# Kernel tuning notes

Measured on AMD Instinct MI355X. Metric: run time of the kernel, lower is better.

Reference implementation:

```python
import jax, jax.numpy as jnp
import numpy as np

BAND_WIDTHS = [16]*20 + [32]*12 + [64]*4 + [65]
B, C, F, T, E = 4, 2, 1025, 2048, 128
MAX_BW = 65
D = C * MAX_BW * 2  # padded feature dim (in_channels * max_bandwidth * reim)
EPS = 1e-5


def _band_meta():
    widths = np.asarray(BAND_WIDTHS, np.int32)
    starts = np.concatenate([[0], np.cumsum(widths)[:-1]]).astype(np.int32)
    nb = len(widths)
    bw_mask = (np.arange(MAX_BW)[None, :] < widths[:, None])  # [nb, MAX_BW]
    # feature order per band is (channel, bw, reim), matching torch view_as_real+reshape
    feat_mask = np.broadcast_to(bw_mask[:, None, :, None], (nb, C, MAX_BW, 2)).reshape(nb, D)
    return starts, widths, feat_mask.astype(np.float32)


def setup_inputs() -> dict:
    key = jax.random.key(0)
    ks = jax.random.split(key, 6)
    starts, widths, feat_mask = _band_meta()
    nb = len(widths)
    fm = jnp.asarray(feat_mask)
    x = jax.random.normal(ks[0], (B, C, F, T, 2), jnp.float32)
    ln_gamma = (1.0 + 0.1 * jax.random.normal(ks[1], (nb, D), jnp.float32)) * fm
    ln_beta = 0.1 * jax.random.normal(ks[2], (nb, D), jnp.float32) * fm
    v = 0.05 * jax.random.normal(ks[3], (nb, E, D), jnp.float32) * fm[:, None, :]
    g = 1.0 + 0.1 * jax.random.normal(ks[4], (nb, E), jnp.float32)
    bias = 0.05 * jax.random.normal(ks[5], (nb, E), jnp.float32)
    return {
        "x": x, "ln_gamma": ln_gamma, "ln_beta": ln_beta, "v": v, "g": g,
        "bias": bias, "band_start": jnp.asarray(starts), "band_width": jnp.asarray(widths),
    }


def reference(x, ln_gamma, ln_beta, v, g, bias, band_start, band_width):
    nb = band_start.shape[0]
    # padded gather of each band's frequency slice
    idx = jnp.clip(band_start[:, None] + jnp.arange(MAX_BW)[None, :], 0, F - 1)  # [nb, MAX_BW]
    xb = jnp.take(x, idx, axis=2)               # [B, C, nb, MAX_BW, T, 2]
    xb = jnp.transpose(xb, (0, 2, 4, 1, 3, 5))  # [B, nb, T, C, MAX_BW, 2]
    xb = xb.reshape(B, nb, T, D)
    bw_mask = (jnp.arange(MAX_BW)[None, :] < band_width[:, None])
    fm = jnp.broadcast_to(bw_mask[:, None, :, None], (nb, C, MAX_BW, 2)).reshape(nb, D).astype(x.dtype)
    m = fm[None, :, None, :]                    # [1, nb, 1, D]
    n = (band_width * C * 2).astype(x.dtype)[None, :, None]  # true norm_in per band
    # masked LayerNorm over the valid (ragged) features of each band
    mean = jnp.sum(xb * m, axis=-1) / n         # [B, nb, T]
    diff = (xb - mean[..., None]) * m
    var = jnp.sum(diff * diff, axis=-1) / n
    xhat = diff * jax.lax.rsqrt(var + EPS)[..., None]
    y = (xhat * ln_gamma[None, :, None, :] + ln_beta[None, :, None, :]) * m
    # weight-normalized Linear: W = g * V / ||V||_row (padded cols of V are zero)
    vnorm = jnp.sqrt(jnp.sum(v * v, axis=-1, keepdims=True))  # [nb, E, 1]
    W = g[..., None] * v / vnorm
    z = jnp.einsum("bntd,ned->bnte", y, W) + bias[:, None, :]  # [B, nb, T, E]
    return z
```

## Files before the change

### kernel.cpp

```cpp
#include <hip/hip_runtime.h>
#include <math.h>

#define NB 37
#define BB 4
#define CC 2
#define FF 1025
#define TT 2048
#define EE 128
#define DD 260
#define EPSF 1e-5f
#define CHS 9

typedef short s16x8 __attribute__((ext_vector_type(8)));
typedef float f32x4 __attribute__((ext_vector_type(4)));

__device__ __forceinline__ unsigned short f2bf(float f) {
    unsigned u = __builtin_bit_cast(unsigned, f);
    unsigned r = (u + 0x7FFFu + ((u >> 16) & 1u)) >> 16;
    return (unsigned short)r;
}

__global__ __launch_bounds__(256) void prep_kernel(
    const float* __restrict__ gamma, const float* __restrict__ beta,
    const float* __restrict__ v, const float* __restrict__ g,
    const float* __restrict__ bias, const int* __restrict__ bwidth,
    unsigned short* __restrict__ ATg, float* __restrict__ s1o, float* __restrict__ s2o)
{
    int bid = blockIdx.x;
    int n   = bid >> 4;
    int eg  = bid & 15;
    int tid = threadIdx.x;
    int el  = tid >> 5;
    int kk  = tid & 31;
    int e   = eg * 8 + el;

    int bw    = bwidth[n];
    int Deff  = 4 * bw;
    int twobw = 2 * bw;
    int nCh   = (Deff + 31) >> 5;

    const float* vp = v + (size_t)(n * EE + e) * DD;

    float sq = 0.f;
    for (int d = kk; d < DD; d += 32) { float val = vp[d]; sq = fmaf(val, val, sq); }
    #pragma unroll
    for (int m = 16; m >= 1; m >>= 1) sq += __shfl_xor(sq, m);

    float rv = g[n * EE + e] * rsqrtf(sq);

    float s1 = 0.f, s2 = 0.f;
    unsigned short* Abase = ATg + (size_t)n * CHS * (EE * 32) + e * 32 + kk;
    for (int ch = 0; ch < nCh; ++ch) {
        int k = ch * 32 + kk;
        float a = 0.f;
        if (k < Deff) {
            int d = (k >= twobw) ? (130 + k - twobw) : k;
            float W = rv * vp[d];
            a = gamma[n * DD + d] * W;
            s1 += a;
            s2 = fmaf(beta[n * DD + d], W, s2);
        }
        Abase[(size_t)ch * (EE * 32)] = f2bf(a);
    }
    #pragma unroll
    for (int m = 16; m >= 1; m >>= 1) { s1 += __shfl_xor(s1, m); s2 += __shfl_xor(s2, m); }
    if (kk == 0) {
        s1o[n * EE + e] = s1;
        s2o[n * EE + e] = s2 + bias[n * EE + e];
    }
}

template <bool PRED>
__device__ __forceinline__ void do_chunk(
    const float* __restrict__ xt, const unsigned* offP,
    const s16x8* __restrict__ Ab, int ch, int nPairs, int ksub,
    f32x4 (&acc)[4][4], float (&sA)[4], float (&qA)[4])
{
    s16x8 bfr[4];
    #pragma unroll
    for (int ni = 0; ni < 4; ++ni) bfr[ni] = Ab[ch * 512 + ni * 64];

    int pb = ch * 16 + (ksub << 2);
    unsigned o[4]; bool val[4];
    #pragma unroll
    for (int j = 0; j < 4; ++j) {
        int p = pb + j;
        val[j] = !PRED || (p < nPairs);
        o[j] = offP[p];
    }

    #pragma unroll
    for (int mi = 0; mi < 4; ++mi) {
        float2 vv[4];
        #pragma unroll
        for (int j = 0; j < 4; ++j) {
            vv[j] = make_float2(0.f, 0.f);
            if (val[j])
                vv[j] = *reinterpret_cast<const float2*>(xt + o[j] + mi * 32);
        }
        float s = sA[mi], q = qA[mi];
        #pragma unroll
        for (int j = 0; j < 4; ++j) {
            s += vv[j].x + vv[j].y;
            q = fmaf(vv[j].x, vv[j].x, q);
            q = fmaf(vv[j].y, vv[j].y, q);
        }
        sA[mi] = s; qA[mi] = q;
        s16x8 af;
        #pragma unroll
        for (int j = 0; j < 4; ++j) {
            af[2 * j]     = (short)f2bf(vv[j].x);
            af[2 * j + 1] = (short)f2bf(vv[j].y);
        }
        #pragma unroll
        for (int ni = 0; ni < 4; ++ni)
            acc[mi][ni] = __builtin_amdgcn_mfma_f32_16x16x32_bf16(
                af, bfr[ni], acc[mi][ni], 0, 0, 0);
    }
}

__global__ __launch_bounds__(256) void fused_kernel(
    const float* __restrict__ x, const int* __restrict__ bstart,
    const int* __restrict__ bwidth,
    const unsigned short* __restrict__ ATg, const float* __restrict__ s1a,
    const float* __restrict__ s2a, float* __restrict__ out)
{
    int bid = blockIdx.x;
    int tt  = bid & 15;
    int n   = (bid >> 4) % NB;
    int b   = bid / (16 * NB);
    int t0  = tt * 128;
    int f0  = bstart[n];
    int bw  = bwidth[n];
    int nPairs = 2 * bw;
    int Deff   = 4 * bw;

    int tid  = threadIdx.x;
    int lane = tid & 63;
    int l15  = lane & 15;
    int ksub = lane >> 4;

    __shared__ unsigned offP[CHS * 16];

    if (tid < CHS * 16) {
        unsigned off = 0;
        if (tid < nPairs) {
            int c = (tid >= bw) ? 1 : 0;
            int w = tid - c * bw;
            off = (unsigned)(((b * CC + c) * FF + f0 + w) * (TT * 2));
        }
        offP[tid] = off;
    }
    __syncthreads();

    int wv    = tid >> 6;
    int twave = t0 + (wv >> 1) * 64;
    int ewave = (wv & 1) * 64;

    f32x4 acc[4][4];
    #pragma unroll
    for (int mi = 0; mi < 4; ++mi)
        #pragma unroll
        for (int ni = 0; ni < 4; ++ni)
            acc[mi][ni] = (f32x4){0.f, 0.f, 0.f, 0.f};
    float sA[4] = {0.f, 0.f, 0.f, 0.f};
    float qA[4] = {0.f, 0.f, 0.f, 0.f};

    const float* xt = x + (size_t)(twave + l15) * 2;
    const s16x8* Ab = reinterpret_cast<const s16x8*>(
        ATg + (size_t)n * CHS * (EE * 32) + ((ewave + l15) * 32 + ksub * 8));

    int nChF = Deff >> 5;
    int rem  = Deff & 31;

    for (int ch = 0; ch < nChF; ++ch)
        do_chunk<false>(xt, offP, Ab, ch, nPairs, ksub, acc, sA, qA);
    if (rem)
        do_chunk<true>(xt, offP, Ab, nChF, nPairs, ksub, acc, sA, qA);

    float inv = 1.f / (float)Deff;
    float mrow[4][4], rrow[4][4];
    #pragma unroll
    for (int mi = 0; mi < 4; ++mi) {
        float s = sA[mi], q = qA[mi];
        s += __shfl_xor(s, 16); s += __shfl_xor(s, 32);
        q += __shfl_xor(q, 16); q += __shfl_xor(q, 32);
        float mean = s * inv;
        float var  = fmaf(q, inv, -mean * mean);
        float rs   = rsqrtf(var + EPSF);
        #pragma unroll
        for (int j = 0; j < 4; ++j) {
            int src = (ksub << 2) + j;
            mrow[mi][j] = __shfl(mean, src);
            rrow[mi][j] = __shfl(rs, src);
        }
    }

    float s1r[4], s2r[4];
    #pragma unroll
    for (int ni = 0; ni < 4; ++ni) {
        int e = ewave + ni * 16 + l15;
        s1r[ni] = s1a[n * EE + e];
        s2r[ni] = s2a[n * EE + e];
    }
    size_t outRow = ((size_t)(b * NB + n)) * TT;
    #pragma unroll
    for (int mi = 0; mi < 4; ++mi) {
        #pragma unroll
        for (int j = 0; j < 4; ++j) {
            int t = twave + mi * 16 + (ksub << 2) + j;
            float m = mrow[mi][j], r = rrow[mi][j];
            float* op = out + (outRow + t) * EE + ewave + l15;
            #pragma unroll
            for (int ni = 0; ni < 4; ++ni)
                op[ni * 16] = fmaf(r, acc[mi][ni][j] - m * s1r[ni], s2r[ni]);
        }
    }
}

extern "C" void kernel_launch(void* const* d_in, const int* in_sizes, int n_in,
                              void* d_out, int out_size, void* d_ws, size_t ws_size,
                              hipStream_t stream)
{
    const float* x      = (const float*)d_in[0];
    const float* gamma  = (const float*)d_in[1];
    const float* beta   = (const float*)d_in[2];
    const float* v      = (const float*)d_in[3];
    const float* g      = (const float*)d_in[4];
    const float* bias   = (const float*)d_in[5];
    const int*   bstart = (const int*)d_in[6];
    const int*   bwidth = (const int*)d_in[7];
    float* out = (float*)d_out;

    unsigned short* ATg = (unsigned short*)d_ws;
    float* s1  = (float*)(ATg + (size_t)NB * CHS * EE * 32);
    float* s2p = s1 + NB * EE;

    prep_kernel<<<NB * 16, 256, 0, stream>>>(gamma, beta, v, g, bias, bwidth, ATg, s1, s2p);
    fused_kernel<<<BB * NB * 16, 256, 0, stream>>>(x, bstart, bwidth, ATg, s1, s2p, out);
}
```

Before: 94.23 us.

## Specialize fused kernel per band width with double-buffered register prefetch

The fused kernel now dispatches to a template instantiated for each band width (16, 32, 64, 65), so the chunk count is a compile-time constant and the chunk loop is fully unrolled. Input and weight fragments for the next chunk are loaded into a second register buffer while the current chunk is computed, so global-memory latency overlaps the MFMAs. The shared-memory offset table and its barrier are replaced by offsets computed directly from the band start. The cost is higher register pressure from two fragment buffers, which could lower occupancy, plus larger code from four instantiations. The else branch assumes every other band is width 65, which matches the task's band list.

```diff
diff --git a/kernel.cpp b/kernel.cpp
--- a/kernel.cpp
+++ b/kernel.cpp
@@ -70,52 +70,140 @@
     }
 }
 
-template <bool PRED>
-__device__ __forceinline__ void do_chunk(
-    const float* __restrict__ xt, const unsigned* offP,
-    const s16x8* __restrict__ Ab, int ch, int nPairs, int ksub,
-    f32x4 (&acc)[4][4], float (&sA)[4], float (&qA)[4])
-{
-    s16x8 bfr[4];
-    #pragma unroll
-    for (int ni = 0; ni < 4; ++ni) bfr[ni] = Ab[ch * 512 + ni * 64];
-
-    int pb = ch * 16 + (ksub << 2);
-    unsigned o[4]; bool val[4];
+struct Frag {
+    float2 xv[16];
+    s16x8  a[4];
+};
+
+template <int BW>
+__device__ __forceinline__ void load_chunk(
+    int ch, bool tailch, const char* __restrict__ xb,
+    const s16x8* __restrict__ Ab, int ksub, Frag& f)
+{
+    #pragma unroll
+    for (int ni = 0; ni < 4; ++ni)
+        f.a[ni] = Ab[ch * 512 + ni * 64];
+
     #pragma unroll
     for (int j = 0; j < 4; ++j) {
-        int p = pb + j;
-        val[j] = !PRED || (p < nPairs);
-        o[j] = offP[p];
-    }
-
+        int p = ch * 16 + ksub * 4 + j;
+        const char* ap = xb + (size_t)p * 16384
+                       + ((p >= BW) ? (size_t)(FF - BW) * 16384 : (size_t)0);
+        bool valid = !tailch || (ksub * 4 + j) < (2 * BW - ch * 16);
+        #pragma unroll
+        for (int mi = 0; mi < 4; ++mi) {
+            float2 vv = make_float2(0.f, 0.f);
+            if (valid)
+                vv = *reinterpret_cast<const float2*>(ap + mi * 128);
+            f.xv[j * 4 + mi] = vv;
+        }
+    }
+}
+
+__device__ __forceinline__ void compute_chunk(
+    const Frag& f, f32x4 (&acc)[4][4], float (&sA)[4], float (&qA)[4])
+{
     #pragma unroll
     for (int mi = 0; mi < 4; ++mi) {
-        float2 vv[4];
+        float s = 0.f, q = 0.f;
+        s16x8 af;
         #pragma unroll
         for (int j = 0; j < 4; ++j) {
-            vv[j] = make_float2(0.f, 0.f);
-            if (val[j])
-                vv[j] = *reinterpret_cast<const float2*>(xt + o[j] + mi * 32);
-        }
-        float s = sA[mi], q = qA[mi];
-        #pragma unroll
-        for (int j = 0; j < 4; ++j) {
-            s += vv[j].x + vv[j].y;
-            q = fmaf(vv[j].x, vv[j].x, q);
-            q = fmaf(vv[j].y, vv[j].y, q);
-        }
-        sA[mi] = s; qA[mi] = q;
-        s16x8 af;
-        #pragma unroll
-        for (int j = 0; j < 4; ++j) {
-            af[2 * j]     = (short)f2bf(vv[j].x);
-            af[2 * j + 1] = (short)f2bf(vv[j].y);
-        }
+            float2 vv = f.xv[j * 4 + mi];
+            s += vv.x + vv.y;
+            q = fmaf(vv.x, vv.x, q);
+            q = fmaf(vv.y, vv.y, q);
+            af[2 * j]     = (short)f2bf(vv.x);
+            af[2 * j + 1] = (short)f2bf(vv.y);
+        }
+        sA[mi] += s;
+        qA[mi] += q;
         #pragma unroll
         for (int ni = 0; ni < 4; ++ni)
             acc[mi][ni] = __builtin_amdgcn_mfma_f32_16x16x32_bf16(
-                af, bfr[ni], acc[mi][ni], 0, 0, 0);
+                af, f.a[ni], acc[mi][ni], 0, 0, 0);
+    }
+}
+
+template <int BW, bool TAIL>
+__device__ __forceinline__ void run_band(
+    const float* __restrict__ x, const unsigned short* __restrict__ ATg,
+    const float* __restrict__ s1a, const float* __restrict__ s2a,
+    float* __restrict__ out, int b, int n, int t0, int f0, int tid)
+{
+    constexpr int NCHF = (4 * BW) / 32;
+    constexpr int NCH  = NCHF + (TAIL ? 1 : 0);
+
+    int lane = tid & 63;
+    int l15  = lane & 15;
+    int ksub = lane >> 4;
+    int wv    = tid >> 6;
+    int twave = t0 + (wv >> 1) * 64;
+    int ewave = (wv & 1) * 64;
+
+    const char* xb = (const char*)x
+        + ((size_t)(b * 2 * FF + f0)) * 16384
+        + (size_t)(twave + l15) * 8;
+    const s16x8* Ab = reinterpret_cast<const s16x8*>(
+        ATg + (size_t)n * CHS * (EE * 32)) + ((ewave + l15) * 4 + ksub);
+
+    f32x4 acc[4][4];
+    #pragma unroll
+    for (int mi = 0; mi < 4; ++mi)
+        #pragma unroll
+        for (int ni = 0; ni < 4; ++ni)
+            acc[mi][ni] = (f32x4){0.f, 0.f, 0.f, 0.f};
+    float sA[4] = {0.f, 0.f, 0.f, 0.f};
+    float qA[4] = {0.f, 0.f, 0.f, 0.f};
+
+    Frag fr0, fr1;
+    load_chunk<BW>(0, false, xb, Ab, ksub, fr0);
+    #pragma unroll
+    for (int ch = 0; ch < NCH; ++ch) {
+        Frag& cur = (ch & 1) ? fr1 : fr0;
+        Frag& nxt = (ch & 1) ? fr0 : fr1;
+        if (ch + 1 < NCH)
+            load_chunk<BW>(ch + 1, (ch + 1 == NCHF) && TAIL, xb, Ab, ksub, nxt);
+        compute_chunk(cur, acc, sA, qA);
+    }
+
+    constexpr float inv = 1.f / (float)(4 * BW);
+    float mrow[4][4], rrow[4][4];
+    #pragma unroll
+    for (int mi = 0; mi < 4; ++mi) {
+        float s = sA[mi], q = qA[mi];
+        s += __shfl_xor(s, 16); s += __shfl_xor(s, 32);
+        q += __shfl_xor(q, 16); q += __shfl_xor(q, 32);
+        float mean = s * inv;
+        float var  = fmaf(q, inv, -mean * mean);
+        float rs   = rsqrtf(var + EPSF);
+        #pragma unroll
+        for (int j = 0; j < 4; ++j) {
+            int src = (ksub << 2) + j;
+            mrow[mi][j] = __shfl(mean, src);
+            rrow[mi][j] = __shfl(rs, src);
+        }
+    }
+
+    float s1r[4], s2r[4];
+    #pragma unroll
+    for (int ni = 0; ni < 4; ++ni) {
+        int e = ewave + ni * 16 + l15;
+        s1r[ni] = s1a[n * EE + e];
+        s2r[ni] = s2a[n * EE + e];
+    }
+    size_t outRow = ((size_t)(b * NB + n)) * TT;
+    #pragma unroll
+    for (int mi = 0; mi < 4; ++mi) {
+        #pragma unroll
+        for (int j = 0; j < 4; ++j) {
+            int t = twave + mi * 16 + (ksub << 2) + j;
+            float m = mrow[mi][j], r = rrow[mi][j];
+            float* op = out + (outRow + t) * EE + ewave + l15;
+            #pragma unroll
+            for (int ni = 0; ni < 4; ++ni)
+                op[ni * 16] = fmaf(r, acc[mi][ni][j] - m * s1r[ni], s2r[ni]);
+        }
     }
 }
 
@@ -132,90 +220,16 @@
     int t0  = tt * 128;
     int f0  = bstart[n];
     int bw  = bwidth[n];
-    int nPairs = 2 * bw;
-    int Deff   = 4 * bw;
-
-    int tid  = threadIdx.x;
-    int lane = tid & 63;
-    int l15  = lane & 15;
-    int ksub = lane >> 4;
-
-    __shared__ unsigned offP[CHS * 16];
-
-    if (tid < CHS * 16) {
-        unsigned off = 0;
-        if (tid < nPairs) {
-            int c = (tid >= bw) ? 1 : 0;
-            int w = tid - c * bw;
-            off = (unsigned)(((b * CC + c) * FF + f0 + w) * (TT * 2));
-        }
-        offP[tid] = off;
-    }
-    __syncthreads();
-
-    int wv    = tid >> 6;
-    int twave = t0 + (wv >> 1) * 64;
-    int ewave = (wv & 1) * 64;
-
-    f32x4 acc[4][4];
-    #pragma unroll
-    for (int mi = 0; mi < 4; ++mi)
-        #pragma unroll
-        for (int ni = 0; ni < 4; ++ni)
-            acc[mi][ni] = (f32x4){0.f, 0.f, 0.f, 0.f};
-    float sA[4] = {0.f, 0.f, 0.f, 0.f};
-    float qA[4] = {0.f, 0.f, 0.f, 0.f};
-
-    const float* xt = x + (size_t)(twave + l15) * 2;
-    const s16x8* Ab = reinterpret_cast<const s16x8*>(
-        ATg + (size_t)n * CHS * (EE * 32) + ((ewave + l15) * 32 + ksub * 8));
-
-    int nChF = Deff >> 5;
-    int rem  = Deff & 31;
-
-    for (int ch = 0; ch < nChF; ++ch)
-        do_chunk<false>(xt, offP, Ab, ch, nPairs, ksub, acc, sA, qA);
-    if (rem)
-        do_chunk<true>(xt, offP, Ab, nChF, nPairs, ksub, acc, sA, qA);
-
-    float inv = 1.f / (float)Deff;
-    float mrow[4][4], rrow[4][4];
-    #pragma unroll
-    for (int mi = 0; mi < 4; ++mi) {
-        float s = sA[mi], q = qA[mi];
-        s += __shfl_xor(s, 16); s += __shfl_xor(s, 32);
-        q += __shfl_xor(q, 16); q += __shfl_xor(q, 32);
-        float mean = s * inv;
-        float var  = fmaf(q, inv, -mean * mean);
-        float rs   = rsqrtf(var + EPSF);
-        #pragma unroll
-        for (int j = 0; j < 4; ++j) {
-            int src = (ksub << 2) + j;
-            mrow[mi][j] = __shfl(mean, src);
-            rrow[mi][j] = __shfl(rs, src);
-        }
-    }
-
-    float s1r[4], s2r[4];
-    #pragma unroll
-    for (int ni = 0; ni < 4; ++ni) {
-        int e = ewave + ni * 16 + l15;
-        s1r[ni] = s1a[n * EE + e];
-        s2r[ni] = s2a[n * EE + e];
-    }
-    size_t outRow = ((size_t)(b * NB + n)) * TT;
-    #pragma unroll
-    for (int mi = 0; mi < 4; ++mi) {
-        #pragma unroll
-        for (int j = 0; j < 4; ++j) {
-            int t = twave + mi * 16 + (ksub << 2) + j;
-            float m = mrow[mi][j], r = rrow[mi][j];
-            float* op = out + (outRow + t) * EE + ewave + l15;
-            #pragma unroll
-            for (int ni = 0; ni < 4; ++ni)
-                op[ni * 16] = fmaf(r, acc[mi][ni][j] - m * s1r[ni], s2r[ni]);
-        }
-    }
+    int tid = threadIdx.x;
+
+    if (bw == 16)
+        run_band<16, false>(x, ATg, s1a, s2a, out, b, n, t0, f0, tid);
+    else if (bw == 32)
+        run_band<32, false>(x, ATg, s1a, s2a, out, b, n, t0, f0, tid);
+    else if (bw == 64)
+        run_band<64, false>(x, ATg, s1a, s2a, out, b, n, t0, f0, tid);
+    else
+        run_band<65, true>(x, ATg, s1a, s2a, out, b, n, t0, f0, tid);
 }
 
 extern "C" void kernel_launch(void* const* d_in, const int* in_sizes, int n_in,
```

After: 100.0 us. 1.06x slower.

## Stage x tiles into LDS with double-buffered async global_load_lds

Applied to the files above, without the earlier changes.

Replaces direct per-lane global float2 loads of x with async global-to-LDS copies (global_load_lds, 16 B per lane) into a double-buffered shared tile, prefetching the next chunk while MFMAs consume the current one. Block index order is changed so consecutive blocks walk bands first, and launch bounds request 3 blocks per CU. This is meant to give coalesced, wide loads and hide global memory latency. In exchange it uses 32 KB of LDS per block and adds a barrier per chunk, which may limit occupancy.

```diff
diff --git a/kernel.cpp b/kernel.cpp
--- a/kernel.cpp
+++ b/kernel.cpp
@@ -13,6 +13,8 @@
 
 typedef short s16x8 __attribute__((ext_vector_type(8)));
 typedef float f32x4 __attribute__((ext_vector_type(4)));
+typedef const unsigned int __attribute__((address_space(1))) gu32;
+typedef unsigned int __attribute__((address_space(3))) lu32;
 
 __device__ __forceinline__ unsigned short f2bf(float f) {
     unsigned u = __builtin_bit_cast(unsigned, f);
@@ -70,92 +72,55 @@
     }
 }
 
-template <bool PRED>
-__device__ __forceinline__ void do_chunk(
-    const float* __restrict__ xt, const unsigned* offP,
-    const s16x8* __restrict__ Ab, int ch, int nPairs, int ksub,
-    f32x4 (&acc)[4][4], float (&sA)[4], float (&qA)[4])
-{
-    s16x8 bfr[4];
-    #pragma unroll
-    for (int ni = 0; ni < 4; ++ni) bfr[ni] = Ab[ch * 512 + ni * 64];
-
-    int pb = ch * 16 + (ksub << 2);
-    unsigned o[4]; bool val[4];
-    #pragma unroll
-    for (int j = 0; j < 4; ++j) {
-        int p = pb + j;
-        val[j] = !PRED || (p < nPairs);
-        o[j] = offP[p];
-    }
-
-    #pragma unroll
-    for (int mi = 0; mi < 4; ++mi) {
-        float2 vv[4];
-        #pragma unroll
-        for (int j = 0; j < 4; ++j) {
-            vv[j] = make_float2(0.f, 0.f);
-            if (val[j])
-                vv[j] = *reinterpret_cast<const float2*>(xt + o[j] + mi * 32);
-        }
-        float s = sA[mi], q = qA[mi];
-        #pragma unroll
-        for (int j = 0; j < 4; ++j) {
-            s += vv[j].x + vv[j].y;
-            q = fmaf(vv[j].x, vv[j].x, q);
-            q = fmaf(vv[j].y, vv[j].y, q);
-        }
-        sA[mi] = s; qA[mi] = q;
-        s16x8 af;
-        #pragma unroll
-        for (int j = 0; j < 4; ++j) {
-            af[2 * j]     = (short)f2bf(vv[j].x);
-            af[2 * j + 1] = (short)f2bf(vv[j].y);
-        }
-        #pragma unroll
-        for (int ni = 0; ni < 4; ++ni)
-            acc[mi][ni] = __builtin_amdgcn_mfma_f32_16x16x32_bf16(
-                af, bfr[ni], acc[mi][ni], 0, 0, 0);
-    }
-}
-
-__global__ __launch_bounds__(256) void fused_kernel(
+__global__ __launch_bounds__(256, 3) void fused_kernel(
     const float* __restrict__ x, const int* __restrict__ bstart,
     const int* __restrict__ bwidth,
     const unsigned short* __restrict__ ATg, const float* __restrict__ s1a,
     const float* __restrict__ s2a, float* __restrict__ out)
 {
-    int bid = blockIdx.x;
-    int tt  = bid & 15;
-    int n   = (bid >> 4) % NB;
-    int b   = bid / (16 * NB);
-    int t0  = tt * 128;
-    int f0  = bstart[n];
-    int bw  = bwidth[n];
+    int bid  = blockIdx.x;
+    int n    = bid % NB;
+    int rest = bid / NB;
+    int tt   = rest & 15;
+    int b    = rest >> 4;
+    int t0   = tt * 128;
+    int f0   = bstart[n];
+    int bw   = bwidth[n];
     int nPairs = 2 * bw;
     int Deff   = 4 * bw;
-
-    int tid  = threadIdx.x;
-    int lane = tid & 63;
-    int l15  = lane & 15;
-    int ksub = lane >> 4;
-
-    __shared__ unsigned offP[CHS * 16];
-
-    if (tid < CHS * 16) {
-        unsigned off = 0;
-        if (tid < nPairs) {
-            int c = (tid >= bw) ? 1 : 0;
-            int w = tid - c * bw;
-            off = (unsigned)(((b * CC + c) * FF + f0 + w) * (TT * 2));
-        }
-        offP[tid] = off;
-    }
-    __syncthreads();
-
+    int nChF   = Deff >> 5;
+    int remP   = nPairs - nChF * 16;
+    int nChT   = nChF + (remP ? 1 : 0);
+
+    int tid   = threadIdx.x;
+    int lane  = tid & 63;
+    int l15   = lane & 15;
+    int ksub  = lane >> 4;
     int wv    = tid >> 6;
-    int twave = t0 + (wv >> 1) * 64;
+    int tband = (wv >> 1) * 64;
     int ewave = (wv & 1) * 64;
+
+    __shared__ __align__(16) float Xs[2][16 * 256];
+
+    const char* xbase = (const char*)x;
+
+    auto STAGE = [&](int ch, int bufIdx) {
+        #pragma unroll
+        for (int j = 0; j < 4; ++j) {
+            int pl = wv * 4 + j;
+            int p  = ch * 16 + pl;
+            p = (p < nPairs) ? p : (nPairs - 1);
+            int c   = (p >= bw) ? 1 : 0;
+            int row = (b * CC + c) * FF + f0 + (p - c * bw);
+            const char* gsrc = xbase + (size_t)row * 16384 + (size_t)t0 * 8
+                             + (size_t)lane * 16;
+            __builtin_amdgcn_global_load_lds(
+                (gu32*)gsrc, (lu32*)&Xs[bufIdx][pl * 256], 16, 0, 0);
+        }
+    };
+
+    const s16x8* Ab = reinterpret_cast<const s16x8*>(
+        ATg + (size_t)n * CHS * (EE * 32)) + ((ewave + l15) * 4 + ksub);
 
     f32x4 acc[4][4];
     #pragma unroll
@@ -166,17 +131,50 @@
     float sA[4] = {0.f, 0.f, 0.f, 0.f};
     float qA[4] = {0.f, 0.f, 0.f, 0.f};
 
-    const float* xt = x + (size_t)(twave + l15) * 2;
-    const s16x8* Ab = reinterpret_cast<const s16x8*>(
-        ATg + (size_t)n * CHS * (EE * 32) + ((ewave + l15) * 32 + ksub * 8));
-
-    int nChF = Deff >> 5;
-    int rem  = Deff & 31;
-
-    for (int ch = 0; ch < nChF; ++ch)
-        do_chunk<false>(xt, offP, Ab, ch, nPairs, ksub, acc, sA, qA);
-    if (rem)
-        do_chunk<true>(xt, offP, Ab, nChF, nPairs, ksub, acc, sA, qA);
+    STAGE(0, 0);
+    __syncthreads();
+
+    for (int ch = 0; ch < nChT; ++ch) {
+        s16x8 a0 = Ab[ch * 512];
+        s16x8 a1 = Ab[ch * 512 + 64];
+        s16x8 a2 = Ab[ch * 512 + 128];
+        s16x8 a3 = Ab[ch * 512 + 192];
+
+        if (ch + 1 < nChT) STAGE(ch + 1, (ch + 1) & 1);
+
+        const float2* Xp = reinterpret_cast<const float2*>(&Xs[ch & 1][0]);
+        bool tail = (ch == nChF);
+
+        #pragma unroll
+        for (int mi = 0; mi < 4; ++mi) {
+            float2 vv[4];
+            #pragma unroll
+            for (int j = 0; j < 4; ++j)
+                vv[j] = Xp[(4 * ksub + j) * 128 + tband + mi * 16 + l15];
+            if (tail) {
+                #pragma unroll
+                for (int j = 0; j < 4; ++j)
+                    if (4 * ksub + j >= remP) vv[j] = make_float2(0.f, 0.f);
+            }
+            float s = 0.f, q = 0.f;
+            s16x8 af;
+            #pragma unroll
+            for (int j = 0; j < 4; ++j) {
+                s += vv[j].x + vv[j].y;
+                q = fmaf(vv[j].x, vv[j].x, q);
+                q = fmaf(vv[j].y, vv[j].y, q);
+                af[2 * j]     = (short)f2bf(vv[j].x);
+                af[2 * j + 1] = (short)f2bf(vv[j].y);
+            }
+            sA[mi] += s;
+            qA[mi] += q;
+            acc[mi][0] = __builtin_amdgcn_mfma_f32_16x16x32_bf16(af, a0, acc[mi][0], 0, 0, 0);
+            acc[mi][1] = __builtin_amdgcn_mfma_f32_16x16x32_bf16(af, a1, acc[mi][1], 0, 0, 0);
+            acc[mi][2] = __builtin_amdgcn_mfma_f32_16x16x32_bf16(af, a2, acc[mi][2], 0, 0, 0);
+            acc[mi][3] = __builtin_amdgcn_mfma_f32_16x16x32_bf16(af, a3, acc[mi][3], 0, 0, 0);
+        }
+        __syncthreads();
+    }
 
     float inv = 1.f / (float)Deff;
     float mrow[4][4], rrow[4][4];
@@ -208,7 +206,7 @@
     for (int mi = 0; mi < 4; ++mi) {
         #pragma unroll
         for (int j = 0; j < 4; ++j) {
-            int t = twave + mi * 16 + (ksub << 2) + j;
+            int t = t0 + tband + mi * 16 + (ksub << 2) + j;
             float m = mrow[mi][j], r = rrow[mi][j];
             float* op = out + (outRow + t) * EE + ewave + l15;
             #pragma unroll
```

After: 82.29 us. -12.7%, faster.
